# Kernel tuning notes

Hardware: AMD Instinct MI355X
Metric: run time of the kernel (lower is better)

Reference implementation:

```python
import jax, jax.numpy as jnp
import numpy as np

B, S, HID = 2, 2048, 1024
NH, DK = 16, 64  # head_size, att_size = hidden // head_size
SCALE = DK ** (-0.5)
NEG = -1000000000.0


def setup_inputs() -> dict:
    key = jax.random.key(0)
    ks = jax.random.split(key, 8)
    return {
        "q": jax.random.normal(ks[0], (B, S, HID), dtype=jnp.float32),
        "k": jax.random.normal(ks[1], (B, S, HID), dtype=jnp.float32),
        "v": jax.random.normal(ks[2], (B, S, HID), dtype=jnp.float32),
        "mask": jax.random.randint(ks[3], (B, S, S), 0, 2, dtype=jnp.int32),
        "Wq": jax.random.normal(ks[4], (HID, HID), dtype=jnp.float32) * (HID ** -0.5),
        "Wk": jax.random.normal(ks[5], (HID, HID), dtype=jnp.float32) * (HID ** -0.5),
        "Wv": jax.random.normal(ks[6], (HID, HID), dtype=jnp.float32) * (HID ** -0.5),
        "Wo": jax.random.normal(ks[7], (HID, HID), dtype=jnp.float32) * (HID ** -0.5),
    }


def reference(q, k, v, mask, Wq, Wk, Wv, Wo):
    b, s, _ = q.shape
    # project and split heads: [B, H, S, dk]
    qh = (q @ Wq).reshape(b, s, NH, DK).transpose(0, 2, 1, 3)
    kh = (k @ Wk).reshape(b, s, NH, DK).transpose(0, 2, 1, 3)
    vh = (v @ Wv).reshape(b, s, NH, DK).transpose(0, 2, 1, 3)
    # scaled QK^T + additive mask (masked_fill with -1e9 where mask is truthy)
    scores = jnp.einsum('bhqd,bhkd->bhqk', qh * SCALE, kh)
    scores = jnp.where(mask[:, None].astype(bool), NEG, scores)
    att = jax.nn.softmax(scores, axis=-1)  # dropout_rate=0.0 -> identity
    out = jnp.einsum('bhqk,bhkd->bhqd', att, vh)
    out = out.transpose(0, 2, 1, 3).reshape(b, s, NH * DK)
    return out @ Wo
```

## Files before the change

### kernel.cpp

```cpp
#include <hip/hip_runtime.h>
#include <stdint.h>

typedef __bf16 bf16x8 __attribute__((ext_vector_type(8)));
typedef float f32x4 __attribute__((ext_vector_type(4)));
typedef unsigned int u32v2 __attribute__((ext_vector_type(2)));
typedef unsigned short us_t;
typedef unsigned short us4 __attribute__((ext_vector_type(4)));

constexpr int B_ = 2, S_ = 2048, HID_ = 1024, NH_ = 16, DK_ = 64;
constexpr float SC2_ = 0.125f * 1.44269504089f;
constexpr float MFIX_ = 16.0f;

#if __has_builtin(__builtin_amdgcn_exp2f)
#define EX2(x) __builtin_amdgcn_exp2f(x)
#else
#define EX2(x) exp2f(x)
#endif

__device__ __forceinline__ us_t f2b(float f) {
  unsigned u = __builtin_bit_cast(unsigned, f);
  u = u + 0x7FFFu + ((u >> 16) & 1u);
  return (us_t)(u >> 16);
}

__device__ __forceinline__ unsigned pk2(float a, float b) {
  union { __bf16 h[2]; unsigned u; } x;
  x.h[0] = (__bf16)a; x.h[1] = (__bf16)b;
  return x.u;
}

__device__ __forceinline__ void gl_lds16(const void* g, void* l) {
  __builtin_amdgcn_global_load_lds((const __attribute__((address_space(1))) void*)g,
                                   (__attribute__((address_space(3))) void*)l, 16, 0, 0);
}

__global__ void k_wt(const float* __restrict__ Wq, const float* __restrict__ Wk,
                     const float* __restrict__ Wv, const float* __restrict__ Wo,
                     us_t* __restrict__ wt) {
  const float* Wsrc;
  switch (blockIdx.z) {
    case 0: Wsrc = Wq; break;
    case 1: Wsrc = Wk; break;
    case 2: Wsrc = Wv; break;
    default: Wsrc = Wo; break;
  }
  us_t* dst = wt + (size_t)blockIdx.z * HID_ * HID_;
  __shared__ float t[32][33];
  int tx = threadIdx.x, ty = threadIdx.y;
  int k0 = blockIdx.y * 32, n0 = blockIdx.x * 32;
#pragma unroll
  for (int i = 0; i < 4; i++)
    t[ty + 8 * i][tx] = Wsrc[(size_t)(k0 + ty + 8 * i) * HID_ + n0 + tx];
  __syncthreads();
#pragma unroll
  for (int i = 0; i < 4; i++)
    dst[(size_t)(n0 + ty + 8 * i) * HID_ + k0 + tx] = f2b(t[tx][ty + 8 * i]);
}

__global__ void k_cvt(const float* __restrict__ q, const float* __restrict__ k,
                      const float* __restrict__ v, us_t* __restrict__ dstbase) {
  const float* src = (blockIdx.z == 0) ? q : (blockIdx.z == 1 ? k : v);
  us_t* dst = dstbase + (size_t)blockIdx.z * B_ * S_ * HID_;
  size_t i = ((size_t)blockIdx.x * blockDim.x + threadIdx.x) * 8;
  float4 a = *(const float4*)(src + i);
  float4 b = *(const float4*)(src + i + 4);
  union { uint4 u; us_t s[8]; } o;
  o.s[0] = f2b(a.x); o.s[1] = f2b(a.y); o.s[2] = f2b(a.z); o.s[3] = f2b(a.w);
  o.s[4] = f2b(b.x); o.s[5] = f2b(b.y); o.s[6] = f2b(b.z); o.s[7] = f2b(b.w);
  *(uint4*)(dst + i) = o.u;
}

__global__ void k_mask(const int* __restrict__ mask, unsigned long long* __restrict__ bits) {
  size_t t = (size_t)blockIdx.x * 256 + threadIdx.x;
  int m = mask[t];
  unsigned long long bal = __ballot(m != 0);
  if ((threadIdx.x & 63) == 0) bits[t >> 6] = bal;
}

template <int OUT>
__global__ __launch_bounds__(256) void k_gemm(const us_t* __restrict__ A0,
                                              const us_t* __restrict__ Bt0,
                                              us_t* __restrict__ Cb,
                                              float* __restrict__ Cf,
                                              us_t* __restrict__ Cv) {
  const int z = blockIdx.z;
  const us_t* A = A0 + (size_t)z * 4096 * 1024;
  const us_t* Bt = Bt0 + (size_t)z * 1024 * 1024;
  __shared__ __attribute__((aligned(16))) us_t At[128 * 32];
  __shared__ __attribute__((aligned(16))) us_t Bts[128 * 32];
  const int tid = threadIdx.x, w = tid >> 6, lane = tid & 63;
  const int m0 = blockIdx.y * 128, n0 = blockIdx.x * 128;
  const int wrow = (w >> 1) * 64, wcol = (w & 1) * 64;
  f32x4 acc[4][4];
#pragma unroll
  for (int i = 0; i < 4; i++)
#pragma unroll
    for (int j = 0; j < 4; j++) acc[i][j] = (f32x4){0.f, 0.f, 0.f, 0.f};

  for (int kb = 0; kb < 1024; kb += 32) {
    __syncthreads();
#pragma unroll
    for (int t = 0; t < 2; t++) {
      const int id = w + t * 4;
      const int r0 = id * 16;
      const us_t* ga = A + (size_t)(m0 + r0 + (lane >> 2)) * 1024 + kb + (lane & 3) * 8;
      gl_lds16(ga, &At[r0 * 32]);
      const us_t* gb = Bt + (size_t)(n0 + r0 + (lane >> 2)) * 1024 + kb + (lane & 3) * 8;
      gl_lds16(gb, &Bts[r0 * 32]);
    }
    __syncthreads();
    bf16x8 af[4], bfv[4];
#pragma unroll
    for (int i = 0; i < 4; i++)
      af[i] = *(const bf16x8*)&At[(wrow + i * 16 + (lane & 15)) * 32 + (lane >> 4) * 8];
#pragma unroll
    for (int j = 0; j < 4; j++)
      bfv[j] = *(const bf16x8*)&Bts[(wcol + j * 16 + (lane & 15)) * 32 + (lane >> 4) * 8];
#pragma unroll
    for (int i = 0; i < 4; i++)
#pragma unroll
      for (int j = 0; j < 4; j++)
        acc[i][j] = __builtin_amdgcn_mfma_f32_16x16x32_bf16(af[i], bfv[j], acc[i][j], 0, 0, 0);
  }
#pragma unroll
  for (int i = 0; i < 4; i++)
#pragma unroll
    for (int j = 0; j < 4; j++) {
      if (OUT == 3 && z == 2) {
        const int col = n0 + wcol + j * 16 + (lane & 15);
        const int row0 = m0 + wrow + i * 16 + ((lane >> 4) << 2);
        us4 val = {f2b(acc[i][j][0]), f2b(acc[i][j][1]), f2b(acc[i][j][2]), f2b(acc[i][j][3])};
        *(us4*)&Cv[((size_t)((row0 >> 11) << 10) + col) * 2048 + (row0 & 2047)] = val;
      } else {
#pragma unroll
        for (int r = 0; r < 4; r++) {
          const int row = m0 + wrow + i * 16 + (lane >> 4) * 4 + r;
          const int col = n0 + wcol + j * 16 + (lane & 15);
          const float v = acc[i][j][r];
          if (OUT == 1) Cf[(size_t)row * 1024 + col] = v;
          else Cb[(size_t)z * 4096 * 1024 + (size_t)row * 1024 + col] = f2b(v);
        }
      }
    }
}

__global__ __launch_bounds__(256) void k_attn(const us_t* __restrict__ Qh,
                                              const us_t* __restrict__ Kh,
                                              const us_t* __restrict__ Vt,
                                              const unsigned long long* __restrict__ mbits,
                                              us_t* __restrict__ O) {
  const int tid = threadIdx.x, w = tid >> 6, lane = tid & 63;
  const int g = lane >> 4, q15 = lane & 15;
  const int qb0 = blockIdx.x * 64;
  const int bh = blockIdx.y, b = bh >> 4, h = bh & 15;
  __shared__ __attribute__((aligned(16))) us_t Ktile[2][4096];
  __shared__ __attribute__((aligned(16))) us_t Vtile[2][4096];
  __shared__ __attribute__((aligned(16))) us_t Pl[4][1024];

  const us_t* Khead = Kh + (size_t)b * S_ * HID_ + h * 64;
  const us_t* Vthead = Vt + ((size_t)b * 1024 + h * 64) * 2048;

  const int qrow = qb0 + w * 16 + q15;
  const us_t* Qbase = Qh + (size_t)b * S_ * HID_ + h * 64 + (size_t)qrow * HID_;
  const bf16x8 qf0 = *(const bf16x8*)&Qbase[g * 8];
  const bf16x8 qf1 = *(const bf16x8*)&Qbase[32 + g * 8];

  const unsigned long long* mrow = mbits + ((size_t)b * S_ + qrow) * 32;

  float l_r = 0.f;
  f32x4 o[4];
#pragma unroll
  for (int dt = 0; dt < 4; dt++) o[dt] = (f32x4){0.f, 0.f, 0.f, 0.f};

  const int ci0 = tid, ci1 = 256 + tid;
  const int r0 = ci0 >> 3, c0 = (ci0 & 7) ^ (r0 & 7);
  const int r1 = ci1 >> 3, c1 = (ci1 & 7) ^ (r1 & 7);
  const us_t* kp0 = Khead + (size_t)r0 * HID_ + c0 * 8;
  const us_t* kp1 = Khead + (size_t)r1 * HID_ + c1 * 8;
  const us_t* vp0 = Vthead + (size_t)r0 * 2048 + c0 * 8;
  const us_t* vp1 = Vthead + (size_t)r1 * 2048 + c1 * 8;

#define STAGE(bufsel)                              \
  do {                                             \
    gl_lds16(kp0, &Ktile[bufsel][ci0 * 8]);        \
    gl_lds16(kp1, &Ktile[bufsel][ci1 * 8]);        \
    gl_lds16(vp0, &Vtile[bufsel][ci0 * 8]);        \
    gl_lds16(vp1, &Vtile[bufsel][ci1 * 8]);        \
    kp0 += 64 * HID_; kp1 += 64 * HID_;            \
    vp0 += 64; vp1 += 64;                          \
  } while (0)

  STAGE(0);
  unsigned long long word_next = mrow[0];

  char* const Plw = (char*)&Pl[w][0];
  const int qx = (q15 & 7) << 4;
  const int rx = q15 & 7;

  for (int kv = 0; kv < 32; kv++) {
    const int cur = kv & 1;
    const unsigned long long word = word_next;
    if (kv < 31) {
      STAGE(cur ^ 1);
      asm volatile("s_waitcnt vmcnt(4)" ::: "memory");
    } else {
      asm volatile("s_waitcnt vmcnt(0)" ::: "memory");
    }
    __builtin_amdgcn_s_barrier();
    if (kv < 31) word_next = mrow[kv + 1];

    f32x4 sa[4];
#pragma unroll
    for (int ct = 0; ct < 4; ct++) {
      const int krow = ct * 16 + q15;
      const bf16x8 kf0 = *(const bf16x8*)&Ktile[cur][krow * 64 + ((g ^ rx) << 3)];
      const bf16x8 kf1 = *(const bf16x8*)&Ktile[cur][krow * 64 + (((4 + g) ^ rx) << 3)];
      f32x4 s = (f32x4){0.f, 0.f, 0.f, 0.f};
      s = __builtin_amdgcn_mfma_f32_16x16x32_bf16(kf0, qf0, s, 0, 0, 0);
      s = __builtin_amdgcn_mfma_f32_16x16x32_bf16(kf1, qf1, s, 0, 0, 0);
      sa[ct] = s;
    }

    float p[16];
#pragma unroll
    for (int ct = 0; ct < 4; ct++) {
      const unsigned wct = (unsigned)(word >> (16 * ct + 4 * g));
#pragma unroll
      for (int r = 0; r < 4; r++) {
        const float s = ((wct >> r) & 1u) ? -__builtin_inff()
                                          : __builtin_fmaf(sa[ct][r], SC2_, -MFIX_);
        const float e = EX2(s);
        p[ct * 4 + r] = e;
        l_r += e;
      }
    }

#pragma unroll
    for (int ct = 0; ct < 4; ct++) {
      u32v2 pw = (u32v2){pk2(p[ct * 4 + 0], p[ct * 4 + 1]), pk2(p[ct * 4 + 2], p[ct * 4 + 3])};
      *(u32v2*)(Plw + q15 * 128 + ((ct * 32 + 8 * g) ^ qx)) = pw;
    }
    const bf16x8 pa0 = *(const bf16x8*)(Plw + q15 * 128 + ((16 * g) ^ qx));
    const bf16x8 pa1 = *(const bf16x8*)(Plw + q15 * 128 + ((64 + 16 * g) ^ qx));

#pragma unroll
    for (int dt = 0; dt < 4; dt++) {
      const int vrow = dt * 16 + q15;
      const bf16x8 vf0 = *(const bf16x8*)&Vtile[cur][vrow * 64 + ((g ^ rx) << 3)];
      const bf16x8 vf1 = *(const bf16x8*)&Vtile[cur][vrow * 64 + (((4 + g) ^ rx) << 3)];
      o[dt] = __builtin_amdgcn_mfma_f32_16x16x32_bf16(vf0, pa0, o[dt], 0, 0, 0);
      o[dt] = __builtin_amdgcn_mfma_f32_16x16x32_bf16(vf1, pa1, o[dt], 0, 0, 0);
    }

    asm volatile("s_waitcnt lgkmcnt(0)" ::: "memory");
    __builtin_amdgcn_sched_barrier(0);
    __builtin_amdgcn_s_barrier();
  }
#undef STAGE

  l_r += __shfl_xor(l_r, 16);
  l_r += __shfl_xor(l_r, 32);
  const float inv = 1.0f / l_r;
#pragma unroll
  for (int dt = 0; dt < 4; dt++) {
    u32v2 ow = (u32v2){pk2(o[dt][0] * inv, o[dt][1] * inv), pk2(o[dt][2] * inv, o[dt][3] * inv)};
    *(u32v2*)(Plw + q15 * 128 + ((dt * 32 + 8 * g) ^ qx)) = ow;
  }
  const int q2 = lane >> 2, seg = lane & 3;
  const int qx2 = (q2 & 7) << 4;
  const uint4 ov0 = *(const uint4*)(Plw + q2 * 128 + ((seg * 16) ^ qx2));
  const uint4 ov1 = *(const uint4*)(Plw + q2 * 128 + ((64 + seg * 16) ^ qx2));
  us_t* orow = &O[(size_t)(b * S_ + qb0 + w * 16 + q2) * HID_ + h * 64];
  *(uint4*)&orow[seg * 8] = ov0;
  *(uint4*)&orow[32 + seg * 8] = ov1;
}

extern "C" void kernel_launch(void* const* d_in, const int* in_sizes, int n_in,
                              void* d_out, int out_size, void* d_ws, size_t ws_size,
                              hipStream_t stream) {
  const float* q = (const float*)d_in[0];
  const float* k = (const float*)d_in[1];
  const float* v = (const float*)d_in[2];
  const int* mask = (const int*)d_in[3];
  const float* Wq = (const float*)d_in[4];
  const float* Wk = (const float*)d_in[5];
  const float* Wv = (const float*)d_in[6];
  const float* Wo = (const float*)d_in[7];

  us_t* wt = (us_t*)d_ws;
  us_t* qkvb = wt + (size_t)4 * 1048576;
  us_t* proj = qkvb + (size_t)3 * 4194304;
  us_t* vtg = proj + (size_t)2 * 4194304;
  unsigned long long* mb = (unsigned long long*)(proj + (size_t)3 * 4194304);
  us_t* oat = (us_t*)(mb + 131072);

  k_wt<<<dim3(32, 32, 4), dim3(32, 8), 0, stream>>>(Wq, Wk, Wv, Wo, wt);
  k_cvt<<<dim3(2048, 1, 3), 256, 0, stream>>>(q, k, v, qkvb);
  k_mask<<<dim3(32768), 256, 0, stream>>>(mask, mb);
  k_gemm<3><<<dim3(8, 32, 3), 256, 0, stream>>>(qkvb, wt, proj, nullptr, vtg);
  k_attn<<<dim3(32, 32), 256, 0, stream>>>(proj, proj + (size_t)4194304, vtg, mb, oat);
  k_gemm<1><<<dim3(8, 32, 1), 256, 0, stream>>>(oat, wt + (size_t)3 * 1048576,
                                                nullptr, (float*)d_out, nullptr);
}
```

Baseline: 278.9 us.

## Double-buffer LDS tiles in projection GEMM to overlap global loads with MFMA

The projection GEMM now uses two LDS buffers per operand and prefetches the next K-slab with direct global-to-LDS loads while computing on the current one. Manual vmcnt waits and barriers replace the two __syncthreads per iteration, and load addresses are precomputed as incrementing pointers. This is meant to hide global memory latency behind MFMA work, at the cost of twice the LDS footprint and hand-placed wait counts that must match the number of outstanding loads.

```diff
diff --git a/kernel.cpp b/kernel.cpp
--- a/kernel.cpp
+++ b/kernel.cpp
@@ -86,8 +86,8 @@
   const int z = blockIdx.z;
   const us_t* A = A0 + (size_t)z * 4096 * 1024;
   const us_t* Bt = Bt0 + (size_t)z * 1024 * 1024;
-  __shared__ __attribute__((aligned(16))) us_t At[128 * 32];
-  __shared__ __attribute__((aligned(16))) us_t Bts[128 * 32];
+  __shared__ __attribute__((aligned(16))) us_t At[2][128 * 32];
+  __shared__ __attribute__((aligned(16))) us_t Bts[2][128 * 32];
   const int tid = threadIdx.x, w = tid >> 6, lane = tid & 63;
   const int m0 = blockIdx.y * 128, n0 = blockIdx.x * 128;
   const int wrow = (w >> 1) * 64, wcol = (w & 1) * 64;
@@ -97,31 +97,53 @@
 #pragma unroll
     for (int j = 0; j < 4; j++) acc[i][j] = (f32x4){0.f, 0.f, 0.f, 0.f};
 
-  for (int kb = 0; kb < 1024; kb += 32) {
-    __syncthreads();
-#pragma unroll
-    for (int t = 0; t < 2; t++) {
-      const int id = w + t * 4;
-      const int r0 = id * 16;
-      const us_t* ga = A + (size_t)(m0 + r0 + (lane >> 2)) * 1024 + kb + (lane & 3) * 8;
-      gl_lds16(ga, &At[r0 * 32]);
-      const us_t* gb = Bt + (size_t)(n0 + r0 + (lane >> 2)) * 1024 + kb + (lane & 3) * 8;
-      gl_lds16(gb, &Bts[r0 * 32]);
-    }
-    __syncthreads();
+  const int sr0 = w * 16 + (lane >> 2);
+  const int sr1 = (w + 4) * 16 + (lane >> 2);
+  const int sc = (lane & 3) * 8;
+  const us_t* ap0 = A + (size_t)(m0 + sr0) * 1024 + sc;
+  const us_t* ap1 = A + (size_t)(m0 + sr1) * 1024 + sc;
+  const us_t* bp0 = Bt + (size_t)(n0 + sr0) * 1024 + sc;
+  const us_t* bp1 = Bt + (size_t)(n0 + sr1) * 1024 + sc;
+
+#define GSTAGE(buf_)                                   \
+  do {                                                 \
+    gl_lds16(ap0, &At[buf_][(w * 16) * 32]);           \
+    gl_lds16(bp0, &Bts[buf_][(w * 16) * 32]);          \
+    gl_lds16(ap1, &At[buf_][((w + 4) * 16) * 32]);     \
+    gl_lds16(bp1, &Bts[buf_][((w + 4) * 16) * 32]);    \
+    ap0 += 32; ap1 += 32; bp0 += 32; bp1 += 32;        \
+  } while (0)
+
+  GSTAGE(0);
+  for (int kb = 0; kb < 32; kb++) {
+    const int cur = kb & 1;
+    if (kb < 31) {
+      GSTAGE(cur ^ 1);
+      asm volatile("s_waitcnt vmcnt(4)" ::: "memory");
+    } else {
+      asm volatile("s_waitcnt vmcnt(0)" ::: "memory");
+    }
+    __builtin_amdgcn_s_barrier();
+
     bf16x8 af[4], bfv[4];
 #pragma unroll
     for (int i = 0; i < 4; i++)
-      af[i] = *(const bf16x8*)&At[(wrow + i * 16 + (lane & 15)) * 32 + (lane >> 4) * 8];
+      af[i] = *(const bf16x8*)&At[cur][(wrow + i * 16 + (lane & 15)) * 32 + (lane >> 4) * 8];
 #pragma unroll
     for (int j = 0; j < 4; j++)
-      bfv[j] = *(const bf16x8*)&Bts[(wcol + j * 16 + (lane & 15)) * 32 + (lane >> 4) * 8];
+      bfv[j] = *(const bf16x8*)&Bts[cur][(wcol + j * 16 + (lane & 15)) * 32 + (lane >> 4) * 8];
 #pragma unroll
     for (int i = 0; i < 4; i++)
 #pragma unroll
       for (int j = 0; j < 4; j++)
         acc[i][j] = __builtin_amdgcn_mfma_f32_16x16x32_bf16(af[i], bfv[j], acc[i][j], 0, 0, 0);
+
+    asm volatile("s_waitcnt lgkmcnt(0)" ::: "memory");
+    __builtin_amdgcn_sched_barrier(0);
+    __builtin_amdgcn_s_barrier();
   }
+#undef GSTAGE
+
 #pragma unroll
   for (int i = 0; i < 4; i++)
 #pragma unroll
```

New measurement: 287.4 us. 1.03x slower.
